# Performance work log

Hardware: AMD Instinct MI355X
Metric: run time of the kernel (lower is better)

Reference implementation:

```python
import jax, jax.numpy as jnp
import numpy as np

B, C, H, W = 8, 512, 64, 64
K = 8  # shrink factor: qk channels = C//K, v channels = C//2


def conv1x1(x, w, b):
    # x: [B,C_in,H,W], w: [C_out,C_in], b: [C_out]  (1x1 conv == channel matmul)
    return jnp.einsum('bchw,oc->bohw', x, w) + b[None, :, None, None]


def maxpool2x2(x):
    b, c, h, w = x.shape
    return x.reshape(b, c, h // 2, 2, w // 2, 2).max(axis=(3, 5))


def setup_inputs() -> dict:
    key = jax.random.key(0)
    ks = jax.random.split(key, 9)
    Cqk, Cv = C // K, C // 2
    sc = lambda fan_in: 1.0 / np.sqrt(fan_in)
    return {
        'x': jax.random.normal(ks[0], (B, C, H, W), jnp.float32),
        'Wf': jax.random.normal(ks[1], (Cqk, C), jnp.float32) * sc(C),
        'bf': jnp.zeros((Cqk,), jnp.float32),
        'Wg': jax.random.normal(ks[2], (Cqk, C), jnp.float32) * sc(C),
        'bg': jnp.zeros((Cqk,), jnp.float32),
        'Wh': jax.random.normal(ks[3], (Cv, C), jnp.float32) * sc(C),
        'bh': jnp.zeros((Cv,), jnp.float32),
        'Wv': jax.random.normal(ks[4], (C, Cv), jnp.float32) * sc(Cv),
        'bv': jnp.zeros((C,), jnp.float32),
        'gamma': jnp.float32(0.5),
    }


def reference(x, Wf, bf, Wg, bg, Wh, bh, Wv, bv, gamma):
    b, c, h, w = x.shape
    f = conv1x1(x, Wf, bf).reshape(b, c // K, h * w)          # [B, C/K, HW]
    g = maxpool2x2(conv1x1(x, Wg, bg))                         # [B, C/K, H/2, W/2]
    v = maxpool2x2(conv1x1(x, Wh, bh))                         # [B, C/2, H/2, W/2]
    hwp = (h // 2) * (w // 2)
    g = g.reshape(b, c // K, hwp)
    v = v.reshape(b, c // 2, hwp)
    # s[b, n, m] = sum_c f[b,c,n] g[b,c,m]; softmax over m (no scaling, per SAGAN)
    s = jnp.einsum('bcn,bcm->bnm', f, g)                       # [B, HW, HW']
    beta = jax.nn.softmax(s, axis=-1)
    o = jnp.einsum('bcm,bnm->bcn', v, beta).reshape(b, c // 2, h, w)
    return gamma * conv1x1(o, Wv, bv) + x
```

## Files before the change

kernel.cpp:

```cpp
#include <hip/hip_runtime.h>
#include <cstddef>

typedef __attribute__((ext_vector_type(4))) float f32x4;
typedef __attribute__((ext_vector_type(16))) float f32x16;
typedef __attribute__((ext_vector_type(8))) short bf16x8;

#define MFMA16(A, B, C) __builtin_amdgcn_mfma_f32_16x16x32_bf16(A, B, C, 0, 0, 0)
#define MFMA32(A, B, C) __builtin_amdgcn_mfma_f32_32x32x16_bf16(A, B, C, 0, 0, 0)

__device__ __forceinline__ unsigned short f2bf(float f) {
  unsigned u = __float_as_uint(f);
  u += 0x7fffu + ((u >> 16) & 1u);
  return (unsigned short)(u >> 16);
}
__device__ __forceinline__ float bf2f(unsigned short s) {
  return __uint_as_float(((unsigned)s) << 16);
}

__device__ __forceinline__ void cvt_split8(float4 a, float4 b, bf16x8* H, bf16x8* L) {
  float v[8] = {a.x, a.y, a.z, a.w, b.x, b.y, b.z, b.w};
  unsigned hh[4], ll[4];
  #pragma unroll
  for (int p = 0; p < 4; ++p) {
    unsigned short h0 = f2bf(v[2 * p]), h1 = f2bf(v[2 * p + 1]);
    hh[p] = (unsigned)h0 | ((unsigned)h1 << 16);
    unsigned short l0 = f2bf(v[2 * p] - bf2f(h0));
    unsigned short l1 = f2bf(v[2 * p + 1] - bf2f(h1));
    ll[p] = (unsigned)l0 | ((unsigned)l1 << 16);
  }
  uint4 uh; uh.x = hh[0]; uh.y = hh[1]; uh.z = hh[2]; uh.w = hh[3];
  uint4 ul; ul.x = ll[0]; ul.y = ll[1]; ul.z = ll[2]; ul.w = ll[3];
  *H = *(bf16x8*)&uh;
  *L = *(bf16x8*)&ul;
}

__device__ __forceinline__ bf16x8 cvt_hi8(float4 a, float4 b) {
  float v[8] = {a.x, a.y, a.z, a.w, b.x, b.y, b.z, b.w};
  unsigned hh[4];
  #pragma unroll
  for (int p = 0; p < 4; ++p)
    hh[p] = (unsigned)f2bf(v[2 * p]) | ((unsigned)f2bf(v[2 * p + 1]) << 16);
  uint4 uh; uh.x = hh[0]; uh.y = hh[1]; uh.z = hh[2]; uh.w = hh[3];
  return *(bf16x8*)&uh;
}


__global__ void prep_k(const float* __restrict__ Wf, const float* __restrict__ Wg,
                       const float* __restrict__ Wh, const float* __restrict__ Wv,
                       unsigned short* __restrict__ wfh, unsigned short* __restrict__ wfl,
                       unsigned short* __restrict__ wgh, unsigned short* __restrict__ wgl,
                       unsigned short* __restrict__ whb, unsigned short* __restrict__ wvb) {
  int i = blockIdx.x * 256 + threadIdx.x;
  if (i < 65536) {
    int ii = i & 32767;
    int j = ii & 7, slot = (ii >> 3) & 63, q = slot & 15, qt2 = slot >> 4;
    int kt = (ii >> 9) & 15, oct = ii >> 13;
    const float* src = (i < 32768) ? Wf : Wg;
    unsigned short* dh = (i < 32768) ? wfh : wgh;
    unsigned short* dl = (i < 32768) ? wfl : wgl;
    float v = src[(oct * 16 + q) * 512 + kt * 32 + qt2 * 8 + j];
    unsigned short h = f2bf(v);
    dh[ii] = h; dl[ii] = f2bf(v - bf2f(h));
  } else if (i < 196608) {
    int ii = i - 65536;
    int j = ii & 7, slot = (ii >> 3) & 63, q = slot & 15, qt2 = slot >> 4;
    int kt = (ii >> 9) & 15, oct = ii >> 13;
    whb[ii] = f2bf(Wh[(oct * 16 + q) * 512 + kt * 32 + qt2 * 8 + j]);
  } else if (i < 327680) {
    int ii = i - 196608;
    int j = ii & 7, slot = (ii >> 3) & 63, q = slot & 15, qt2 = slot >> 4;
    int kt = (ii >> 9) & 7, oct = ii >> 12;
    wvb[ii] = f2bf(Wv[(oct * 16 + q) * 256 + kt * 32 + qt2 * 8 + j]);
  }
}


#define LOADX64(CN) { _Pragma("unroll") \
  for (int t_ = 0; t_ < 32; ++t_) vv[t_] = xbase[(size_t)((CN) * 64 + kq + t_) * 4096]; }
#define STOREX64(BUF) { _Pragma("unroll") \
  for (int i_ = 0; i_ < 8; ++i_) { \
    float4 wv_; wv_.x = vv[4*i_]; wv_.y = vv[4*i_+1]; wv_.z = vv[4*i_+2]; wv_.w = vv[4*i_+3]; \
    *(float4*)&xs[BUF][nloc][kq + 4 * i_] = wv_; } }

__global__ __launch_bounds__(256, 2)
void conv_all(const float* __restrict__ x,
              const unsigned short* __restrict__ wfh_, const unsigned short* __restrict__ wfl_,
              const unsigned short* __restrict__ wgh_, const unsigned short* __restrict__ wgl_,
              const unsigned short* __restrict__ whb_,
              const float* __restrict__ bf_, const float* __restrict__ bg_,
              const float* __restrict__ bh_,
              unsigned short* __restrict__ fhi, unsigned short* __restrict__ flo,
              unsigned short* __restrict__ ghi, unsigned short* __restrict__ glo,
              unsigned short* __restrict__ vp)
{
  __shared__ __align__(16) float xs[2][128][65];
  const int bid = blockIdx.x;
  const int b = bid & 7;
  const int idx = bid >> 3;
  const int role = idx & 1;
  const int hp = idx >> 1;
  const int n0 = hp * 128;
  const int tid = threadIdx.x, w = tid >> 6, lane = tid & 63, q = lane & 15, qt = lane >> 4;
  const int nloc = tid & 127;
  const int kq = (tid >> 7) * 32;
  const float* xbase = x + (size_t)(b * 512) * 4096 + n0 + nloc;
  float vv[32];

  if (role == 0) {
    f32x4 accf[2][4], accg[2][4];
    #pragma unroll
    for (int nt = 0; nt < 2; ++nt)
      #pragma unroll
      for (int ot = 0; ot < 4; ++ot) {
        accf[nt][ot] = (f32x4){0.f, 0.f, 0.f, 0.f};
        accg[nt][ot] = (f32x4){0.f, 0.f, 0.f, 0.f};
      }
    LOADX64(0) STOREX64(0)
    __syncthreads();
    for (int cc = 0; cc < 8; ++cc) {
      const int cur = cc & 1;
      if (cc < 7) LOADX64(cc + 1)
      #pragma unroll
      for (int kh = 0; kh < 2; ++kh) {
        const int kt = cc * 2 + kh;
        bf16x8 Ah[2], Al[2];
        #pragma unroll
        for (int nt = 0; nt < 2; ++nt) {
          int row = w * 32 + nt * 16 + q;
          float4 a0 = *(const float4*)&xs[cur][row][kh * 32 + qt * 8];
          float4 a1 = *(const float4*)&xs[cur][row][kh * 32 + qt * 8 + 4];
          cvt_split8(a0, a1, &Ah[nt], &Al[nt]);
        }
        {
          bf16x8 Bh[4], Bl[4];
          #pragma unroll
          for (int ot = 0; ot < 4; ++ot) {
            size_t wb = ((size_t)(ot * 16 + kt) << 9) + lane * 8;
            Bh[ot] = *(const bf16x8*)(wfh_ + wb);
            Bl[ot] = *(const bf16x8*)(wfl_ + wb);
          }
          #pragma unroll
          for (int nt = 0; nt < 2; ++nt)
            #pragma unroll
            for (int ot = 0; ot < 4; ++ot) {
              accf[nt][ot] = MFMA16(Ah[nt], Bh[ot], accf[nt][ot]);
              accf[nt][ot] = MFMA16(Ah[nt], Bl[ot], accf[nt][ot]);
              accf[nt][ot] = MFMA16(Al[nt], Bh[ot], accf[nt][ot]);
            }
        }
        {
          bf16x8 Bh[4], Bl[4];
          #pragma unroll
          for (int ot = 0; ot < 4; ++ot) {
            size_t wb = ((size_t)(ot * 16 + kt) << 9) + lane * 8;
            Bh[ot] = *(const bf16x8*)(wgh_ + wb);
            Bl[ot] = *(const bf16x8*)(wgl_ + wb);
          }
          #pragma unroll
          for (int nt = 0; nt < 2; ++nt)
            #pragma unroll
            for (int ot = 0; ot < 4; ++ot) {
              accg[nt][ot] = MFMA16(Ah[nt], Bh[ot], accg[nt][ot]);
              accg[nt][ot] = MFMA16(Ah[nt], Bl[ot], accg[nt][ot]);
              accg[nt][ot] = MFMA16(Al[nt], Bh[ot], accg[nt][ot]);
            }
        }
      }
      if (cc < 7) STOREX64(cur ^ 1)
      __syncthreads();
    }
    #pragma unroll
    for (int nt = 0; nt < 2; ++nt)
      #pragma unroll
      for (int ot = 0; ot < 4; ++ot)
        #pragma unroll
        for (int r = 0; r < 4; ++r) {
          float v = accf[nt][ot][r] + bf_[ot * 16 + q];
          unsigned short h = f2bf(v);
          size_t o = (((size_t)(b * 128 + hp * 4 + w) * 4 + ot) * 64 +
                      (q >> 3) * 32 + nt * 16 + qt * 4 + r) * 8 + (q & 7);
          fhi[o] = h;
          flo[o] = f2bf(v - bf2f(h));
        }
    float (*pl)[67] = (float(*)[67])&xs[0][0][0];
    #pragma unroll
    for (int nt = 0; nt < 2; ++nt)
      #pragma unroll
      for (int ot = 0; ot < 4; ++ot)
        #pragma unroll
        for (int r = 0; r < 4; ++r)
          pl[w * 32 + nt * 16 + qt * 4 + r][ot * 16 + q] = accg[nt][ot][r];
    __syncthreads();
    const int c = tid & 63;
    #pragma unroll
    for (int it = 0; it < 8; ++it) {
      int wp = (tid >> 6) + it * 4;
      float v = fmaxf(fmaxf(pl[2 * wp][c], pl[2 * wp + 1][c]),
                      fmaxf(pl[64 + 2 * wp][c], pl[65 + 2 * wp][c])) + bg_[c];
      unsigned short h = f2bf(v);
      size_t o = (((size_t)(b * 32 + hp) * 4 + (c >> 4)) * 64 +
                  ((c >> 3) & 1) * 32 + wp) * 8 + (c & 7);
      ghi[o] = h;
      glo[o] = f2bf(v - bf2f(h));
    }
  } else {
    f32x4 acc[2][16];
    #pragma unroll
    for (int nt = 0; nt < 2; ++nt)
      #pragma unroll
      for (int ot = 0; ot < 16; ++ot) acc[nt][ot] = (f32x4){0.f, 0.f, 0.f, 0.f};
    LOADX64(0) STOREX64(0)
    __syncthreads();
    for (int cc = 0; cc < 8; ++cc) {
      const int cur = cc & 1;
      if (cc < 7) LOADX64(cc + 1)
      #pragma unroll
      for (int kh = 0; kh < 2; ++kh) {
        const int kt = cc * 2 + kh;
        bf16x8 A_[2];
        #pragma unroll
        for (int nt = 0; nt < 2; ++nt) {
          int row = w * 32 + nt * 16 + q;
          float4 a0 = *(const float4*)&xs[cur][row][kh * 32 + qt * 8];
          float4 a1 = *(const float4*)&xs[cur][row][kh * 32 + qt * 8 + 4];
          A_[nt] = cvt_hi8(a0, a1);
        }
        #pragma unroll
        for (int oh = 0; oh < 2; ++oh) {
          bf16x8 B_[8];
          #pragma unroll
          for (int ot = 0; ot < 8; ++ot)
            B_[ot] = *(const bf16x8*)(whb_ + ((size_t)((oh * 8 + ot) * 16 + kt) << 9) + lane * 8);
          #pragma unroll
          for (int nt = 0; nt < 2; ++nt)
            #pragma unroll
            for (int ot = 0; ot < 8; ++ot)
              acc[nt][oh * 8 + ot] = MFMA16(A_[nt], B_[ot], acc[nt][oh * 8 + ot]);
        }
      }
      if (cc < 7) STOREX64(cur ^ 1)
      __syncthreads();
    }
    float (*pl)[67] = (float(*)[67])&xs[0][0][0];
    #pragma unroll
    for (int oh = 0; oh < 4; ++oh) {
      if (oh) __syncthreads();
      #pragma unroll
      for (int nt = 0; nt < 2; ++nt)
        #pragma unroll
        for (int ot4 = 0; ot4 < 4; ++ot4)
          #pragma unroll
          for (int r = 0; r < 4; ++r)
            pl[w * 32 + nt * 16 + qt * 4 + r][ot4 * 16 + q] = acc[nt][oh * 4 + ot4][r];
      __syncthreads();
      const int wp = tid & 31;
      #pragma unroll
      for (int it = 0; it < 8; ++it) {
        int cc2 = (tid >> 5) + it * 8;
        int cv = oh * 64 + cc2;
        float v = fmaxf(fmaxf(pl[2 * wp][cc2], pl[2 * wp + 1][cc2]),
                        fmaxf(pl[64 + 2 * wp][cc2], pl[65 + 2 * wp][cc2])) + bh_[cv];
        size_t o = (((size_t)(b * 16 + (cv >> 4)) * 32 + hp) * 64 +
                    (wp >> 3) * 16 + (cv & 15)) * 8 + (wp & 7);
        vp[o] = f2bf(v);
      }
    }
  }
}


#define PROW 264

__global__ __launch_bounds__(256, 2)
void attn_mfma(const unsigned short* __restrict__ f_, const unsigned short* __restrict__ fl_,
               const unsigned short* __restrict__ g_, const unsigned short* __restrict__ gl_,
               const unsigned short* __restrict__ vp, unsigned short* __restrict__ oT)
{
  __shared__ __align__(16) unsigned short PB[64 * PROW];
  __shared__ float redm[4][2][32], reds[4][2][32];
  const int b = blockIdx.x & 7, bx = blockIdx.x >> 3;
  const int tid = threadIdx.x, w = tid >> 6, lane = tid & 63;
  const int q32 = lane & 31, hl = lane >> 5;
  const int q16 = lane & 15, qt = lane >> 4;

  bf16x8 Fh[2][4], Fl[2][4];
  #pragma unroll
  for (int qt2 = 0; qt2 < 2; ++qt2) {
    size_t fb = ((size_t)(b * 128 + bx * 2 + qt2) << 11) + lane * 8;
    #pragma unroll
    for (int s = 0; s < 4; ++s) {
      Fh[qt2][s] = *(const bf16x8*)(f_ + fb + (s << 9));
      Fl[qt2][s] = *(const bf16x8*)(fl_ + fb + (s << 9));
    }
  }

  float M0 = -3.0e38f, M1 = -3.0e38f;
  float Mp[4], Sp[4];
  #pragma unroll
  for (int qs = 0; qs < 4; ++qs) { Mp[qs] = -3.0e38f; Sp[qs] = 0.f; }
  f32x4 oacc[4][4];
  #pragma unroll
  for (int c4 = 0; c4 < 4; ++c4)
    #pragma unroll
    for (int qs = 0; qs < 4; ++qs) oacc[c4][qs] = (f32x4){0.f, 0.f, 0.f, 0.f};
  const size_t vroot = ((size_t)(b * 16 + w * 4) * 32) * 512 + lane * 8;

#define VLD(C4, KS) (*(const bf16x8*)(vp + vroot + ((size_t)((C4) * 32 + mc * 8 + (KS)) << 9)))
#define LOADVA(KS) { va0 = VLD(0, KS); va1 = VLD(1, KS); va2 = VLD(2, KS); va3 = VLD(3, KS); }
#define LOADVB(KS) { vb0 = VLD(0, KS); vb1 = VLD(1, KS); vb2 = VLD(2, KS); vb3 = VLD(3, KS); }
#define PVMFMA(KS, V0, V1, V2, V3) { \
  bf16x8 pb0 = *(const bf16x8*)&PB[q16 * PROW + (KS) * 32 + qt * 8]; \
  bf16x8 pb1 = *(const bf16x8*)&PB[(16 + q16) * PROW + (KS) * 32 + qt * 8]; \
  bf16x8 pb2 = *(const bf16x8*)&PB[(32 + q16) * PROW + (KS) * 32 + qt * 8]; \
  bf16x8 pb3 = *(const bf16x8*)&PB[(48 + q16) * PROW + (KS) * 32 + qt * 8]; \
  oacc[0][0] = MFMA16(V0, pb0, oacc[0][0]); oacc[1][0] = MFMA16(V1, pb0, oacc[1][0]); \
  oacc[2][0] = MFMA16(V2, pb0, oacc[2][0]); oacc[3][0] = MFMA16(V3, pb0, oacc[3][0]); \
  oacc[0][1] = MFMA16(V0, pb1, oacc[0][1]); oacc[1][1] = MFMA16(V1, pb1, oacc[1][1]); \
  oacc[2][1] = MFMA16(V2, pb1, oacc[2][1]); oacc[3][1] = MFMA16(V3, pb1, oacc[3][1]); \
  oacc[0][2] = MFMA16(V0, pb2, oacc[0][2]); oacc[1][2] = MFMA16(V1, pb2, oacc[1][2]); \
  oacc[2][2] = MFMA16(V2, pb2, oacc[2][2]); oacc[3][2] = MFMA16(V3, pb2, oacc[3][2]); \
  oacc[0][3] = MFMA16(V0, pb3, oacc[0][3]); oacc[1][3] = MFMA16(V1, pb3, oacc[1][3]); \
  oacc[2][3] = MFMA16(V2, pb3, oacc[2][3]); oacc[3][3] = MFMA16(V3, pb3, oacc[3][3]); }

  #pragma unroll 1
  for (int mc = 0; mc < 4; ++mc) {
    f32x16 sa0t0 = {}, sa0t1 = {}, sa1t0 = {}, sa1t1 = {};
    __builtin_amdgcn_s_setprio(1);
    #pragma unroll
    for (int t = 0; t < 2; ++t) {
      size_t gb = ((size_t)(b * 32 + mc * 8 + w * 2 + t) << 11) + lane * 8;
      bf16x8 Gh[4], Gl[4];
      #pragma unroll
      for (int s = 0; s < 4; ++s) {
        Gh[s] = *(const bf16x8*)(g_ + gb + (s << 9));
        Gl[s] = *(const bf16x8*)(gl_ + gb + (s << 9));
      }
      f32x16* s0 = t ? &sa0t1 : &sa0t0;
      f32x16* s1 = t ? &sa1t1 : &sa1t0;
      #pragma unroll
      for (int s = 0; s < 4; ++s) {
        *s0 = MFMA32(Gh[s], Fh[0][s], *s0);
        *s0 = MFMA32(Gh[s], Fl[0][s], *s0);
        *s0 = MFMA32(Gl[s], Fh[0][s], *s0);
        *s1 = MFMA32(Gh[s], Fh[1][s], *s1);
        *s1 = MFMA32(Gh[s], Fl[1][s], *s1);
        *s1 = MFMA32(Gl[s], Fh[1][s], *s1);
      }
    }
    __builtin_amdgcn_s_setprio(0);

    bf16x8 va0, va1, va2, va3, vb0, vb1, vb2, vb3;
    LOADVA(0)

    float mx0 = -3.0e38f, mx1 = -3.0e38f;
    #pragma unroll
    for (int r = 0; r < 16; ++r) {
      mx0 = fmaxf(mx0, fmaxf(sa0t0[r], sa0t1[r]));
      mx1 = fmaxf(mx1, fmaxf(sa1t0[r], sa1t1[r]));
    }
    mx0 = fmaxf(mx0, __shfl_xor(mx0, 32));
    mx1 = fmaxf(mx1, __shfl_xor(mx1, 32));
    if (lane < 32) { redm[w][0][lane] = mx0; redm[w][1][lane] = mx1; }
    __syncthreads();
    float gmx0 = fmaxf(fmaxf(redm[0][0][q32], redm[1][0][q32]), fmaxf(redm[2][0][q32], redm[3][0][q32]));
    float gmx1 = fmaxf(fmaxf(redm[0][1][q32], redm[1][1][q32]), fmaxf(redm[2][1][q32], redm[3][1][q32]));
    float Mn0 = fmaxf(M0, gmx0), Mn1 = fmaxf(M1, gmx1);
    M0 = Mn0; M1 = Mn1;

    float rfp[4];
    #pragma unroll
    for (int qs = 0; qs < 4; ++qs) {
      int hq = qs >> 1, cq = (qs & 1) * 16 + q16;
      float gm = fmaxf(fmaxf(redm[0][hq][cq], redm[1][hq][cq]),
                       fmaxf(redm[2][hq][cq], redm[3][hq][cq]));
      float Mn = fmaxf(Mp[qs], gm);
      rfp[qs] = __expf(Mp[qs] - Mn);
      Mp[qs] = Mn;
    }

    float cs0 = 0.f, cs1 = 0.f;
    #pragma unroll
    for (int r = 0; r < 16; ++r) {
      float p;
      p = __expf(sa0t0[r] - Mn0); sa0t0[r] = p; cs0 += p;
      p = __expf(sa0t1[r] - Mn0); sa0t1[r] = p; cs0 += p;
      p = __expf(sa1t0[r] - Mn1); sa1t0[r] = p; cs1 += p;
      p = __expf(sa1t1[r] - Mn1); sa1t1[r] = p; cs1 += p;
    }
    cs0 += __shfl_xor(cs0, 32);
    cs1 += __shfl_xor(cs1, 32);
    if (lane < 32) { reds[w][0][lane] = cs0; reds[w][1][lane] = cs1; }

    #pragma unroll
    for (int j = 0; j < 4; ++j) {
      uint2 pk;
      pk.x = (unsigned)f2bf(sa0t0[4*j+0]) | ((unsigned)f2bf(sa0t0[4*j+1]) << 16);
      pk.y = (unsigned)f2bf(sa0t0[4*j+2]) | ((unsigned)f2bf(sa0t0[4*j+3]) << 16);
      *(uint2*)&PB[q32 * PROW + w * 64 + j * 8 + hl * 4] = pk;
      pk.x = (unsigned)f2bf(sa0t1[4*j+0]) | ((unsigned)f2bf(sa0t1[4*j+1]) << 16);
      pk.y = (unsigned)f2bf(sa0t1[4*j+2]) | ((unsigned)f2bf(sa0t1[4*j+3]) << 16);
      *(uint2*)&PB[q32 * PROW + w * 64 + 32 + j * 8 + hl * 4] = pk;
      pk.x = (unsigned)f2bf(sa1t0[4*j+0]) | ((unsigned)f2bf(sa1t0[4*j+1]) << 16);
      pk.y = (unsigned)f2bf(sa1t0[4*j+2]) | ((unsigned)f2bf(sa1t0[4*j+3]) << 16);
      *(uint2*)&PB[(32 + q32) * PROW + w * 64 + j * 8 + hl * 4] = pk;
      pk.x = (unsigned)f2bf(sa1t1[4*j+0]) | ((unsigned)f2bf(sa1t1[4*j+1]) << 16);
      pk.y = (unsigned)f2bf(sa1t1[4*j+2]) | ((unsigned)f2bf(sa1t1[4*j+3]) << 16);
      *(uint2*)&PB[(32 + q32) * PROW + w * 64 + 32 + j * 8 + hl * 4] = pk;
    }
    __syncthreads();

    #pragma unroll
    for (int qs = 0; qs < 4; ++qs) {
      int hq = qs >> 1, cq = (qs & 1) * 16 + q16;
      float ct = reds[0][hq][cq] + reds[1][hq][cq] + reds[2][hq][cq] + reds[3][hq][cq];
      Sp[qs] = (mc == 0) ? ct : Sp[qs] * rfp[qs] + ct;
    }

    if (mc > 0) {
      #pragma unroll
      for (int c4 = 0; c4 < 4; ++c4)
        #pragma unroll
        for (int qs = 0; qs < 4; ++qs) oacc[c4][qs] *= rfp[qs];
    }
    LOADVB(1)
    __builtin_amdgcn_s_setprio(1);
    #pragma unroll
    for (int kp = 0; kp < 4; ++kp) {
      PVMFMA(2 * kp, va0, va1, va2, va3)
      if (2 * kp + 2 < 8) LOADVA(2 * kp + 2)
      PVMFMA(2 * kp + 1, vb0, vb1, vb2, vb3)
      if (2 * kp + 3 < 8) LOADVB(2 * kp + 3)
    }
    __builtin_amdgcn_s_setprio(0);
  }

  __syncthreads();
  float rinv[4];
  #pragma unroll
  for (int qs = 0; qs < 4; ++qs) rinv[qs] = 1.0f / Sp[qs];
  #pragma unroll
  for (int c4 = 0; c4 < 4; ++c4)
    #pragma unroll
    for (int qs = 0; qs < 4; ++qs) {
      uint2 pk;
      pk.x = (unsigned)f2bf(oacc[c4][qs][0] * rinv[qs]) | ((unsigned)f2bf(oacc[c4][qs][1] * rinv[qs]) << 16);
      pk.y = (unsigned)f2bf(oacc[c4][qs][2] * rinv[qs]) | ((unsigned)f2bf(oacc[c4][qs][3] * rinv[qs]) << 16);
      *(uint2*)&PB[(qs * 16 + q16) * PROW + w * 64 + c4 * 16 + qt * 4] = pk;
    }
  __syncthreads();
  const size_t obase = (size_t)(b * 256 + bx * 4) * 4096;
  #pragma unroll
  for (int it = 0; it < 8; ++it) {
    int u = it * 256 + tid;
    int so = u * 8;
    int ntl = so >> 12;
    int rem = so & 4095;
    int ks = rem >> 9;
    int slot = (rem >> 3) & 63;
    int qq = slot & 15, cg = slot >> 4;
    uint4 val = *(const uint4*)&PB[(ntl * 16 + qq) * PROW + ks * 32 + cg * 8];
    *(uint4*)(oT + obase + so) = val;
  }
}


__global__ __launch_bounds__(256)
void conv_final(const unsigned short* __restrict__ A, const unsigned short* __restrict__ W,
                const float* __restrict__ bias, float* __restrict__ out,
                const float* __restrict__ resid, const float* __restrict__ gamma_p)
{
  const int bid = blockIdx.x;
  const int b = bid & 7;
  const int idx = bid >> 3;
  const int n0 = (idx & 31) * 128;
  const int oc0 = (idx >> 5) * 128;
  const int tid = threadIdx.x, w = tid >> 6, lane = tid & 63, q = lane & 15, qt = lane >> 4;

  f32x4 acc[2][8];
  #pragma unroll
  for (int nt = 0; nt < 2; ++nt)
    #pragma unroll
    for (int ot = 0; ot < 8; ++ot) acc[nt][ot] = (f32x4){0.f, 0.f, 0.f, 0.f};

  #pragma unroll
  for (int ks = 0; ks < 8; ++ks) {
    bf16x8 A_[2], B_[8];
    #pragma unroll
    for (int nt = 0; nt < 2; ++nt)
      A_[nt] = *(const bf16x8*)(A + (((size_t)(b * 256 + (n0 >> 4) + w * 2 + nt) * 8 + ks) << 9) + lane * 8);
    #pragma unroll
    for (int ot = 0; ot < 8; ++ot)
      B_[ot] = *(const bf16x8*)(W + (((size_t)((oc0 >> 4) + ot) * 8 + ks) << 9) + lane * 8);
    #pragma unroll
    for (int nt = 0; nt < 2; ++nt)
      #pragma unroll
      for (int ot = 0; ot < 8; ++ot)
        acc[nt][ot] = MFMA16(A_[nt], B_[ot], acc[nt][ot]);
  }

  const float gm = gamma_p[0];
  #pragma unroll
  for (int ot = 0; ot < 8; ++ot) {
    int oc = oc0 + ot * 16 + q;
    float bs = bias[oc];
    #pragma unroll
    for (int nt = 0; nt < 2; ++nt) {
      int n = n0 + w * 32 + nt * 16 + qt * 4;
      size_t o = ((size_t)(b * 512) + oc) * 4096 + n;
      float4 rs = *(const float4*)&resid[o];
      float4 ov;
      ov.x = gm * (acc[nt][ot][0] + bs) + rs.x;
      ov.y = gm * (acc[nt][ot][1] + bs) + rs.y;
      ov.z = gm * (acc[nt][ot][2] + bs) + rs.z;
      ov.w = gm * (acc[nt][ot][3] + bs) + rs.w;
      *(float4*)&out[o] = ov;
    }
  }
}


extern "C" void kernel_launch(void* const* d_in, const int* in_sizes, int n_in,
                              void* d_out, int out_size, void* d_ws, size_t ws_size,
                              hipStream_t stream) {
  const float* x     = (const float*)d_in[0];
  const float* Wf    = (const float*)d_in[1];
  const float* bf    = (const float*)d_in[2];
  const float* Wg    = (const float*)d_in[3];
  const float* bg    = (const float*)d_in[4];
  const float* Wh    = (const float*)d_in[5];
  const float* bh    = (const float*)d_in[6];
  const float* Wv    = (const float*)d_in[7];
  const float* bv    = (const float*)d_in[8];
  const float* gamma = (const float*)d_in[9];
  float* out = (float*)d_out;
  char* w = (char*)d_ws;

  unsigned short* fhi = (unsigned short*)(w);
  unsigned short* flo = (unsigned short*)(w + 4194304);
  unsigned short* ghi = (unsigned short*)(w + 8388608);
  unsigned short* glo = (unsigned short*)(w + 9437184);
  unsigned short* vp  = (unsigned short*)(w + 10485760);
  unsigned short* oT  = (unsigned short*)(w + 14680064);
  unsigned short* wfh = (unsigned short*)(w + 31457280);
  unsigned short* wfl = (unsigned short*)(w + 31522816);
  unsigned short* wgh = (unsigned short*)(w + 31588352);
  unsigned short* wgl = (unsigned short*)(w + 31653888);
  unsigned short* whb = (unsigned short*)(w + 31719424);
  unsigned short* wvb = (unsigned short*)(w + 31981568);

  prep_k<<<1280, 256, 0, stream>>>(Wf, Wg, Wh, Wv, wfh, wfl, wgh, wgl, whb, wvb);

  conv_all<<<512, 256, 0, stream>>>(x, wfh, wfl, wgh, wgl, whb,
                                    bf, bg, bh, fhi, flo, ghi, glo, vp);

  attn_mfma<<<512, 256, 0, stream>>>(fhi, flo, ghi, glo, vp, oT);

  conv_final<<<1024, 256, 0, stream>>>(oT, wvb, bv, out, x, gamma);
}
```

Measured before the change: 112.8 us.

## Stage conv input tiles into LDS with direct global_load_lds transfers

The register-staged copy of x tiles (32 global loads into registers, then float4 stores to shared memory) is replaced by `__builtin_amdgcn_global_load_lds`, which writes global data straight into LDS. The LDS tile is reorganised from pixel-major [128][65] to channel-major [64][128] so each wave's load fills contiguous rows. The aim is to drop the 32-float staging array, which lowers register pressure, and to let the next chunk's prefetch proceed without register round-trips. In exchange, the MFMA A-fragment reads become eight scalar LDS loads per fragment instead of two float4 loads. With unpadded 128-float rows, these reads may also hit LDS bank conflicts.

```diff
diff --git a/kernel.cpp b/kernel.cpp
--- a/kernel.cpp
+++ b/kernel.cpp
@@ -75,12 +75,12 @@
 }
 
 
-#define LOADX64(CN) { _Pragma("unroll") \
-  for (int t_ = 0; t_ < 32; ++t_) vv[t_] = xbase[(size_t)((CN) * 64 + kq + t_) * 4096]; }
-#define STOREX64(BUF) { _Pragma("unroll") \
-  for (int i_ = 0; i_ < 8; ++i_) { \
-    float4 wv_; wv_.x = vv[4*i_]; wv_.y = vv[4*i_+1]; wv_.z = vv[4*i_+2]; wv_.w = vv[4*i_+3]; \
-    *(float4*)&xs[BUF][nloc][kq + 4 * i_] = wv_; } }
+#define STAGE(BUF, CN) { _Pragma("unroll") \
+  for (int c_ = 0; c_ < 8; ++c_) { \
+    __builtin_amdgcn_global_load_lds( \
+      (const __attribute__((address_space(1))) unsigned int*)(xg + (size_t)((CN) * 64 + c_ * 2) * 4096), \
+      (__attribute__((address_space(3))) unsigned int*)(&xs[BUF][w * 16 + c_ * 2][0]), \
+      16, 0, 0); } }
 
 __global__ __launch_bounds__(256, 2)
 void conv_all(const float* __restrict__ x,
@@ -93,7 +93,7 @@
               unsigned short* __restrict__ ghi, unsigned short* __restrict__ glo,
               unsigned short* __restrict__ vp)
 {
-  __shared__ __align__(16) float xs[2][128][65];
+  __shared__ __align__(16) float xs[2][64][128];
   const int bid = blockIdx.x;
   const int b = bid & 7;
   const int idx = bid >> 3;
@@ -101,10 +101,7 @@
   const int hp = idx >> 1;
   const int n0 = hp * 128;
   const int tid = threadIdx.x, w = tid >> 6, lane = tid & 63, q = lane & 15, qt = lane >> 4;
-  const int nloc = tid & 127;
-  const int kq = (tid >> 7) * 32;
-  const float* xbase = x + (size_t)(b * 512) * 4096 + n0 + nloc;
-  float vv[32];
+  const float* xg = x + ((size_t)(b * 512 + w * 16 + (lane >> 5)) * 4096) + n0 + (lane & 31) * 4;
 
   if (role == 0) {
     f32x4 accf[2][4], accg[2][4];
@@ -115,20 +112,24 @@
         accf[nt][ot] = (f32x4){0.f, 0.f, 0.f, 0.f};
         accg[nt][ot] = (f32x4){0.f, 0.f, 0.f, 0.f};
       }
-    LOADX64(0) STOREX64(0)
+    STAGE(0, 0)
     __syncthreads();
     for (int cc = 0; cc < 8; ++cc) {
       const int cur = cc & 1;
-      if (cc < 7) LOADX64(cc + 1)
+      if (cc < 7) STAGE(cur ^ 1, cc + 1)
       #pragma unroll
       for (int kh = 0; kh < 2; ++kh) {
         const int kt = cc * 2 + kh;
         bf16x8 Ah[2], Al[2];
         #pragma unroll
         for (int nt = 0; nt < 2; ++nt) {
-          int row = w * 32 + nt * 16 + q;
-          float4 a0 = *(const float4*)&xs[cur][row][kh * 32 + qt * 8];
-          float4 a1 = *(const float4*)&xs[cur][row][kh * 32 + qt * 8 + 4];
+          const int row = w * 32 + nt * 16 + q;
+          float xv[8];
+          #pragma unroll
+          for (int j = 0; j < 8; ++j)
+            xv[j] = xs[cur][kh * 32 + qt * 8 + j][row];
+          float4 a0; a0.x = xv[0]; a0.y = xv[1]; a0.z = xv[2]; a0.w = xv[3];
+          float4 a1; a1.x = xv[4]; a1.y = xv[5]; a1.z = xv[6]; a1.w = xv[7];
           cvt_split8(a0, a1, &Ah[nt], &Al[nt]);
         }
         {
@@ -166,7 +167,6 @@
             }
         }
       }
-      if (cc < 7) STOREX64(cur ^ 1)
       __syncthreads();
     }
     #pragma unroll
@@ -209,20 +209,24 @@
     for (int nt = 0; nt < 2; ++nt)
       #pragma unroll
       for (int ot = 0; ot < 16; ++ot) acc[nt][ot] = (f32x4){0.f, 0.f, 0.f, 0.f};
-    LOADX64(0) STOREX64(0)
+    STAGE(0, 0)
     __syncthreads();
     for (int cc = 0; cc < 8; ++cc) {
       const int cur = cc & 1;
-      if (cc < 7) LOADX64(cc + 1)
+      if (cc < 7) STAGE(cur ^ 1, cc + 1)
       #pragma unroll
       for (int kh = 0; kh < 2; ++kh) {
         const int kt = cc * 2 + kh;
         bf16x8 A_[2];
         #pragma unroll
         for (int nt = 0; nt < 2; ++nt) {
-          int row = w * 32 + nt * 16 + q;
-          float4 a0 = *(const float4*)&xs[cur][row][kh * 32 + qt * 8];
-          float4 a1 = *(const float4*)&xs[cur][row][kh * 32 + qt * 8 + 4];
+          const int row = w * 32 + nt * 16 + q;
+          float xv[8];
+          #pragma unroll
+          for (int j = 0; j < 8; ++j)
+            xv[j] = xs[cur][kh * 32 + qt * 8 + j][row];
+          float4 a0; a0.x = xv[0]; a0.y = xv[1]; a0.z = xv[2]; a0.w = xv[3];
+          float4 a1; a1.x = xv[4]; a1.y = xv[5]; a1.z = xv[6]; a1.w = xv[7];
           A_[nt] = cvt_hi8(a0, a1);
         }
         #pragma unroll
@@ -238,7 +242,6 @@
               acc[nt][oh * 8 + ot] = MFMA16(A_[nt], B_[ot], acc[nt][oh * 8 + ot]);
         }
       }
-      if (cc < 7) STOREX64(cur ^ 1)
       __syncthreads();
     }
     float (*pl)[67] = (float(*)[67])&xs[0][0][0];
```

Measured after the change: 111.3 us. About the same (-1.3%).
